# Kernel tuning notes

Measured on AMD Instinct MI355X. Metric: run time of the kernel, lower is better.

The kernel has to match this reference:

```python
import jax, jax.numpy as jnp
import numpy as np

N = 50000      # nodes
E = 800000     # directed edges (before self-loops)
IN = 128       # input feature dim
HID = 64       # per-head hidden channels (concat=False -> head mean)
H = 4          # attention heads
OUT = 1
NEG_SLOPE = 0.2


def setup_inputs() -> dict:
    key = jax.random.key(0)
    ks = jax.random.split(key, 20)
    def glorot(k, shape, fan):
        return jax.random.normal(k, shape, jnp.float32) * (1.0 / np.sqrt(fan))
    inp = {
        "x": jax.random.normal(ks[0], (N, IN), jnp.float32),
        "edge_index": jax.random.randint(ks[1], (2, E), 0, N, jnp.int32),
        # layer 1
        "W1": glorot(ks[2], (IN, H * HID), IN),
        "a_s1": glorot(ks[3], (H, HID), HID),
        "a_d1": glorot(ks[4], (H, HID), HID),
        "b1": jnp.zeros((HID,), jnp.float32),
        # layer 2
        "W2": glorot(ks[5], (HID, H * HID), HID),
        "a_s2": glorot(ks[6], (H, HID), HID),
        "a_d2": glorot(ks[7], (H, HID), HID),
        "b2": jnp.zeros((HID,), jnp.float32),
        # layer 3
        "W3": glorot(ks[8], (HID, H * HID), HID),
        "a_s3": glorot(ks[9], (H, HID), HID),
        "a_d3": glorot(ks[10], (H, HID), HID),
        "b3": jnp.zeros((HID,), jnp.float32),
        # final linear
        "fc_W": glorot(ks[11], (HID, OUT), HID),
        "fc_b": jnp.zeros((OUT,), jnp.float32),
    }
    return inp


def _gat_layer(x, src, dst, W, a_s, a_d, b):
    """PyG GATConv with concat=False (mean over heads), self-loops already in src/dst."""
    n = x.shape[0]
    h = (x @ W).reshape(n, H, -1)                      # [N,H,C]
    es = jnp.einsum('nhc,hc->nh', h, a_s)              # [N,H] alpha_src per node
    ed = jnp.einsum('nhc,hc->nh', h, a_d)              # [N,H] alpha_dst per node
    e = jax.nn.leaky_relu(es[src] + ed[dst], NEG_SLOPE)  # [E,H] per-edge logits
    # segment softmax over edges sharing the same dst (every node has a self-loop)
    m = jax.ops.segment_max(e, dst, num_segments=n)
    w = jnp.exp(e - m[dst])
    z = jax.ops.segment_sum(w, dst, num_segments=n)
    alpha = w / z[dst]                                  # [E,H]
    out = jax.ops.segment_sum(alpha[:, :, None] * h[src], dst, num_segments=n)  # [N,H,C]
    return out.mean(axis=1) + b                         # concat=False -> head mean + bias


def reference(x, edge_index, W1, a_s1, a_d1, b1, W2, a_s2, a_d2, b2,
              W3, a_s3, a_d3, b3, fc_W, fc_b):
    n = x.shape[0]
    loops = jnp.arange(n, dtype=edge_index.dtype)
    src = jnp.concatenate([edge_index[0], loops])
    dst = jnp.concatenate([edge_index[1], loops])
    gelu = lambda t: jax.nn.gelu(t, approximate=False)  # torch F.gelu default = exact erf
    x = gelu(_gat_layer(x, src, dst, W1, a_s1, a_d1, b1))
    x = gelu(_gat_layer(x, src, dst, W2, a_s2, a_d2, b2))
    x = gelu(_gat_layer(x, src, dst, W3, a_s3, a_d3, b3))
    # dropout is identity in eval mode (deterministic reference)
    return jax.nn.sigmoid(x @ fc_W + fc_b)              # [N,1]
```

## Files before the change

### kernel.cpp

```cpp
#include <hip/hip_runtime.h>
#include <math.h>

#define N_NODES 50000
#define N_EDGES 800000
#define ETOT    (N_EDGES + N_NODES)
#define DIM_IN  128
#define HID     64
#define NHEAD   4
#define HDIM    256
#define NEG_SLOPE 0.2f

typedef __attribute__((ext_vector_type(8))) short bf16x8;
typedef __attribute__((ext_vector_type(4))) float f32x4;

static __device__ __forceinline__ float gelu_exact(float x) {
    return 0.5f * x * (1.0f + erff(x * 0.70710678118654752f));
}
static __device__ __forceinline__ unsigned short f2bf(float f) {
    unsigned u = __float_as_uint(f);
    u = (u + 0x7FFFu + ((u >> 16) & 1u)) >> 16;
    return (unsigned short)u;
}
static __device__ __forceinline__ float b2f(unsigned short us) {
    return __uint_as_float(((unsigned)us) << 16);
}

__global__ void count_kernel(const int* __restrict__ ei, int* __restrict__ counts) {
    int i = blockIdx.x * 256 + threadIdx.x;
    if (i >= ETOT) return;
    int d = (i < N_EDGES) ? ei[N_EDGES + i] : (i - N_EDGES);
    atomicAdd(&counts[d], 1);
}

__global__ void scan1_kernel(const int* __restrict__ counts, int* __restrict__ offs,
                             int* __restrict__ blockSums) {
    __shared__ int s[256];
    int t = threadIdx.x, idx = blockIdx.x * 256 + t;
    int v = (idx < N_NODES) ? counts[idx] : 0;
    s[t] = v; __syncthreads();
    #pragma unroll
    for (int o = 1; o < 256; o <<= 1) {
        int add = (t >= o) ? s[t - o] : 0;
        __syncthreads();
        s[t] += add;
        __syncthreads();
    }
    if (idx < N_NODES) offs[idx] = s[t] - v;
    if (t == 255) blockSums[blockIdx.x] = s[t];
}

__global__ void scan2_kernel(const int* __restrict__ blockSums, int* __restrict__ blockScan, int nb) {
    __shared__ int s[256];
    int t = threadIdx.x;
    int v = (t < nb) ? blockSums[t] : 0;
    s[t] = v; __syncthreads();
    #pragma unroll
    for (int o = 1; o < 256; o <<= 1) {
        int add = (t >= o) ? s[t - o] : 0;
        __syncthreads();
        s[t] += add;
        __syncthreads();
    }
    blockScan[t] = s[t] - v;
}

__global__ void scan3_kernel(int* __restrict__ offs, const int* __restrict__ blockScan) {
    int idx = blockIdx.x * 256 + threadIdx.x;
    if (idx < N_NODES) offs[idx] += blockScan[blockIdx.x];
    if (idx == 0) offs[N_NODES] = ETOT;
}

__global__ void fill_kernel(const int* __restrict__ ei, const int* __restrict__ offs,
                            int* __restrict__ cursor, int* __restrict__ csrc) {
    int i = blockIdx.x * 256 + threadIdx.x;
    if (i >= ETOT) return;
    int s, d;
    if (i < N_EDGES) { s = ei[i]; d = ei[N_EDGES + i]; } else { s = d = i - N_EDGES; }
    int pos = offs[d] + atomicAdd(&cursor[d], 1);
    csrc[pos] = s;
}

__global__ void convx_kernel(const float4* __restrict__ in, ushort4* __restrict__ outp, int n4) {
    int i = blockIdx.x * 256 + threadIdx.x;
    if (i >= n4) return;
    float4 v = in[i];
    ushort4 o;
    o.x = f2bf(v.x); o.y = f2bf(v.y); o.z = f2bf(v.z); o.w = f2bf(v.w);
    outp[i] = o;
}

__global__ void convw_kernel(const float* __restrict__ W1, const float* __restrict__ W2,
                             const float* __restrict__ W3,
                             unsigned short* __restrict__ Wt1, unsigned short* __restrict__ Wt2,
                             unsigned short* __restrict__ Wt3) {
    int t = blockIdx.x * 256 + threadIdx.x;
    if (t < 32768) {
        int k = t >> 8, n = t & 255;
        Wt1[n * DIM_IN + k] = f2bf(W1[t]);
    } else if (t < 49152) {
        int l = t - 32768; int k = l >> 8, n = l & 255;
        Wt2[n * HID + k] = f2bf(W2[l]);
    } else if (t < 65536) {
        int l = t - 49152; int k = l >> 8, n = l & 255;
        Wt3[n * HID + k] = f2bf(W3[l]);
    }
}

template<int K>
__global__ __launch_bounds__(256) void gemm_mfma_kernel(
    const unsigned short* __restrict__ A, const unsigned short* __restrict__ Wt,
    const float* __restrict__ a_s, const float* __restrict__ a_d,
    unsigned short* __restrict__ h_bf, float* __restrict__ es, float* __restrict__ ed,
    int M)
{
    constexpr int KS = K / 32;
    __shared__ unsigned short hstage[64][HDIM + 8];
    const int lane = threadIdx.x & 63;
    const int head = threadIdx.x >> 6;
    const int l15 = lane & 15;
    const int lg  = lane >> 4;
    const int row0 = blockIdx.x * 64;

    bf16x8 bfrag[4][KS];
    #pragma unroll
    for (int n = 0; n < 4; ++n)
        #pragma unroll
        for (int ks = 0; ks < KS; ++ks)
            bfrag[n][ks] = *(const bf16x8*)(Wt + (size_t)(head * 64 + n * 16 + l15) * K + ks * 32 + lg * 8);

    f32x4 acc[4][4];
    #pragma unroll
    for (int m = 0; m < 4; ++m)
        #pragma unroll
        for (int n = 0; n < 4; ++n)
            acc[m][n] = (f32x4){0.f, 0.f, 0.f, 0.f};

    #pragma unroll
    for (int m = 0; m < 4; ++m) {
        int row = row0 + m * 16 + l15;
        if (row >= M) row = M - 1;
        const unsigned short* ap = A + (size_t)row * K + lg * 8;
        #pragma unroll
        for (int ks = 0; ks < KS; ++ks) {
            bf16x8 af = *(const bf16x8*)(ap + ks * 32);
            #pragma unroll
            for (int n = 0; n < 4; ++n)
                acc[m][n] = __builtin_amdgcn_mfma_f32_16x16x32_bf16(af, bfrag[n][ks], acc[m][n], 0, 0, 0);
        }
    }

    float asv[4], adv[4];
    #pragma unroll
    for (int n = 0; n < 4; ++n) {
        asv[n] = a_s[head * 64 + n * 16 + l15];
        adv[n] = a_d[head * 64 + n * 16 + l15];
    }
    #pragma unroll
    for (int m = 0; m < 4; ++m) {
        #pragma unroll
        for (int r = 0; r < 4; ++r) {
            int rloc = m * 16 + lg * 4 + r;
            float ps = 0.f, pd = 0.f;
            #pragma unroll
            for (int n = 0; n < 4; ++n) {
                float v = acc[m][n][r];
                ps += v * asv[n];
                pd += v * adv[n];
                hstage[rloc][head * 64 + n * 16 + l15] = f2bf(v);
            }
            #pragma unroll
            for (int o = 8; o; o >>= 1) { ps += __shfl_xor(ps, o, 64); pd += __shfl_xor(pd, o, 64); }
            int rg = row0 + rloc;
            if (l15 == 0 && rg < M) { es[rg * 4 + head] = ps; ed[rg * 4 + head] = pd; }
        }
    }
    __syncthreads();
    #pragma unroll
    for (int it = 0; it < 8; ++it) {
        int id = threadIdx.x + it * 256;
        int row = id >> 5, c8 = (id & 31) * 8;
        int rg = row0 + row;
        if (rg < M) {
            int4 v = *(const int4*)(&hstage[row][c8]);
            *(int4*)(h_bf + (size_t)rg * HDIM + c8) = v;
        }
    }
}

template<bool LAST>
__global__ __launch_bounds__(256) void gather_kernel(
    const unsigned short* __restrict__ h_bf,
    const float4* __restrict__ es4, const float4* __restrict__ ed4,
    const int* __restrict__ offs, const int* __restrict__ csrc,
    const float* __restrict__ bias,
    const float* __restrict__ fcW, const float* __restrict__ fcb,
    unsigned short* __restrict__ xout_bf, float* __restrict__ out)
{
    __shared__ float wls[4][64][4];
    __shared__ int   sls[4][64];
    const int wv = threadIdx.x >> 6;
    const int lane = threadIdx.x & 63;
    const int w = blockIdx.x * 4 + wv;
    const int hd = lane >> 4;
    const int ch = lane << 2;
    const int beg = offs[w], end = offs[w + 1];
    const float4 edv = ed4[w];

    float4 mx = {-INFINITY, -INFINITY, -INFINITY, -INFINITY};
    for (int i = beg + lane; i < end; i += 64) {
        float4 e = es4[csrc[i]];
        e.x += edv.x; e.y += edv.y; e.z += edv.z; e.w += edv.w;
        e.x = (e.x > 0.f) ? e.x : NEG_SLOPE * e.x;
        e.y = (e.y > 0.f) ? e.y : NEG_SLOPE * e.y;
        e.z = (e.z > 0.f) ? e.z : NEG_SLOPE * e.z;
        e.w = (e.w > 0.f) ? e.w : NEG_SLOPE * e.w;
        mx.x = fmaxf(mx.x, e.x); mx.y = fmaxf(mx.y, e.y);
        mx.z = fmaxf(mx.z, e.z); mx.w = fmaxf(mx.w, e.w);
    }
    #pragma unroll
    for (int o = 32; o; o >>= 1) {
        mx.x = fmaxf(mx.x, __shfl_xor(mx.x, o, 64));
        mx.y = fmaxf(mx.y, __shfl_xor(mx.y, o, 64));
        mx.z = fmaxf(mx.z, __shfl_xor(mx.z, o, 64));
        mx.w = fmaxf(mx.w, __shfl_xor(mx.w, o, 64));
    }

    float4 zac = {0.f, 0.f, 0.f, 0.f};
    float4 acc = {0.f, 0.f, 0.f, 0.f};
    for (int c0 = beg; c0 < end; c0 += 64) {
        int i = c0 + lane;
        float4 wt = {0.f, 0.f, 0.f, 0.f};
        int sidx = 0;
        if (i < end) {
            sidx = csrc[i];
            float4 e = es4[sidx];
            e.x += edv.x; e.y += edv.y; e.z += edv.z; e.w += edv.w;
            e.x = (e.x > 0.f) ? e.x : NEG_SLOPE * e.x;
            e.y = (e.y > 0.f) ? e.y : NEG_SLOPE * e.y;
            e.z = (e.z > 0.f) ? e.z : NEG_SLOPE * e.z;
            e.w = (e.w > 0.f) ? e.w : NEG_SLOPE * e.w;
            wt.x = __expf(e.x - mx.x); wt.y = __expf(e.y - mx.y);
            wt.z = __expf(e.z - mx.z); wt.w = __expf(e.w - mx.w);
        }
        sls[wv][lane] = sidx;
        *(float4*)(&wls[wv][lane][0]) = wt;
        zac.x += wt.x; zac.y += wt.y; zac.z += wt.z; zac.w += wt.w;
        int nb = end - c0; if (nb > 64) nb = 64;
        int j = 0;
        for (; j + 3 < nb; j += 4) {
            int s0 = sls[wv][j], s1 = sls[wv][j + 1], s2 = sls[wv][j + 2], s3 = sls[wv][j + 3];
            float a0 = wls[wv][j][hd],     a1 = wls[wv][j + 1][hd];
            float a2 = wls[wv][j + 2][hd], a3 = wls[wv][j + 3][hd];
            ushort4 u0 = *(const ushort4*)(h_bf + (size_t)s0 * HDIM + ch);
            ushort4 u1 = *(const ushort4*)(h_bf + (size_t)s1 * HDIM + ch);
            ushort4 u2 = *(const ushort4*)(h_bf + (size_t)s2 * HDIM + ch);
            ushort4 u3 = *(const ushort4*)(h_bf + (size_t)s3 * HDIM + ch);
            acc.x += a0 * b2f(u0.x) + a1 * b2f(u1.x) + a2 * b2f(u2.x) + a3 * b2f(u3.x);
            acc.y += a0 * b2f(u0.y) + a1 * b2f(u1.y) + a2 * b2f(u2.y) + a3 * b2f(u3.y);
            acc.z += a0 * b2f(u0.z) + a1 * b2f(u1.z) + a2 * b2f(u2.z) + a3 * b2f(u3.z);
            acc.w += a0 * b2f(u0.w) + a1 * b2f(u1.w) + a2 * b2f(u2.w) + a3 * b2f(u3.w);
        }
        for (; j < nb; ++j) {
            int s = sls[wv][j];
            float a = wls[wv][j][hd];
            ushort4 u = *(const ushort4*)(h_bf + (size_t)s * HDIM + ch);
            acc.x += a * b2f(u.x); acc.y += a * b2f(u.y);
            acc.z += a * b2f(u.z); acc.w += a * b2f(u.w);
        }
    }
    #pragma unroll
    for (int o = 32; o; o >>= 1) {
        zac.x += __shfl_xor(zac.x, o, 64);
        zac.y += __shfl_xor(zac.y, o, 64);
        zac.z += __shfl_xor(zac.z, o, 64);
        zac.w += __shfl_xor(zac.w, o, 64);
    }
    float zz = (hd == 0) ? zac.x : (hd == 1) ? zac.y : (hd == 2) ? zac.z : zac.w;
    float inv = 1.f / zz;
    acc.x *= inv; acc.y *= inv; acc.z *= inv; acc.w *= inv;
    acc.x += __shfl_xor(acc.x, 16, 64); acc.x += __shfl_xor(acc.x, 32, 64);
    acc.y += __shfl_xor(acc.y, 16, 64); acc.y += __shfl_xor(acc.y, 32, 64);
    acc.z += __shfl_xor(acc.z, 16, 64); acc.z += __shfl_xor(acc.z, 32, 64);
    acc.w += __shfl_xor(acc.w, 16, 64); acc.w += __shfl_xor(acc.w, 32, 64);
    if (lane < 16) {
        float4 bv = *(const float4*)(bias + ch);
        float4 r;
        r.x = gelu_exact(0.25f * acc.x + bv.x);
        r.y = gelu_exact(0.25f * acc.y + bv.y);
        r.z = gelu_exact(0.25f * acc.z + bv.z);
        r.w = gelu_exact(0.25f * acc.w + bv.w);
        if (!LAST) {
            ushort4 o4;
            o4.x = f2bf(r.x); o4.y = f2bf(r.y); o4.z = f2bf(r.z); o4.w = f2bf(r.w);
            *(ushort4*)(xout_bf + (size_t)w * HID + ch) = o4;
        } else {
            float p = r.x * fcW[ch] + r.y * fcW[ch + 1] + r.z * fcW[ch + 2] + r.w * fcW[ch + 3];
            #pragma unroll
            for (int o = 8; o; o >>= 1) p += __shfl_xor(p, o, 64);
            if (lane == 0) out[w] = 1.f / (1.f + __expf(-(p + fcb[0])));
        }
    }
}

extern "C" void kernel_launch(void* const* d_in, const int* in_sizes, int n_in,
                              void* d_out, int out_size, void* d_ws, size_t ws_size,
                              hipStream_t stream) {
    const float* x    = (const float*)d_in[0];
    const int*   ei   = (const int*)d_in[1];
    const float* W1   = (const float*)d_in[2];
    const float* as1  = (const float*)d_in[3];
    const float* ad1  = (const float*)d_in[4];
    const float* b1   = (const float*)d_in[5];
    const float* W2   = (const float*)d_in[6];
    const float* as2  = (const float*)d_in[7];
    const float* ad2  = (const float*)d_in[8];
    const float* b2   = (const float*)d_in[9];
    const float* W3   = (const float*)d_in[10];
    const float* as3  = (const float*)d_in[11];
    const float* ad3  = (const float*)d_in[12];
    const float* b3   = (const float*)d_in[13];
    const float* fcW  = (const float*)d_in[14];
    const float* fcb  = (const float*)d_in[15];
    float* out = (float*)d_out;

    char* ws = (char*)d_ws;
    size_t off = 0;
    auto alloc = [&](size_t bytes) -> void* {
        void* p = ws + off;
        off += (bytes + 255) & ~(size_t)255;
        return p;
    };
    unsigned short* h_bf  = (unsigned short*)alloc((size_t)N_NODES * HDIM * 2);
    unsigned short* x_bf  = (unsigned short*)alloc((size_t)N_NODES * DIM_IN * 2);
    unsigned short* xA_bf = (unsigned short*)alloc((size_t)N_NODES * HID * 2);
    unsigned short* xB_bf = (unsigned short*)alloc((size_t)N_NODES * HID * 2);
    unsigned short* Wt1   = (unsigned short*)alloc((size_t)HDIM * DIM_IN * 2);
    unsigned short* Wt2   = (unsigned short*)alloc((size_t)HDIM * HID * 2);
    unsigned short* Wt3   = (unsigned short*)alloc((size_t)HDIM * HID * 2);
    float* esb   = (float*)alloc((size_t)N_NODES * 4 * 4);
    float* edb   = (float*)alloc((size_t)N_NODES * 4 * 4);
    int* offs    = (int*)alloc((size_t)(N_NODES + 1) * 4);
    int* counts  = (int*)alloc((size_t)2 * N_NODES * 4);
    int* cursor  = counts + N_NODES;
    int* bsums   = (int*)alloc(256 * 4);
    int* bscan   = (int*)alloc(256 * 4);
    int* csrc    = (int*)alloc((size_t)ETOT * 4);

    const int NB    = (N_NODES + 255) / 256;
    const int EB    = (ETOT + 255) / 256;
    const int GB    = (N_NODES + 63) / 64;
    const int AGB   = N_NODES / 4;
    const int CXB   = (N_NODES * DIM_IN / 4 + 255) / 256;

    hipMemsetAsync(counts, 0, (size_t)2 * N_NODES * 4, stream);
    count_kernel<<<EB, 256, 0, stream>>>(ei, counts);
    scan1_kernel<<<NB, 256, 0, stream>>>(counts, offs, bsums);
    scan2_kernel<<<1, 256, 0, stream>>>(bsums, bscan, NB);
    scan3_kernel<<<NB, 256, 0, stream>>>(offs, bscan);
    fill_kernel<<<EB, 256, 0, stream>>>(ei, offs, cursor, csrc);

    convx_kernel<<<CXB, 256, 0, stream>>>((const float4*)x, (ushort4*)x_bf, N_NODES * DIM_IN / 4);
    convw_kernel<<<256, 256, 0, stream>>>(W1, W2, W3, Wt1, Wt2, Wt3);

    gemm_mfma_kernel<DIM_IN><<<GB, 256, 0, stream>>>(x_bf, Wt1, as1, ad1, h_bf, esb, edb, N_NODES);
    gather_kernel<false><<<AGB, 256, 0, stream>>>(h_bf, (const float4*)esb, (const float4*)edb,
                                                  offs, csrc, b1, fcW, fcb, xA_bf, out);
    gemm_mfma_kernel<HID><<<GB, 256, 0, stream>>>(xA_bf, Wt2, as2, ad2, h_bf, esb, edb, N_NODES);
    gather_kernel<false><<<AGB, 256, 0, stream>>>(h_bf, (const float4*)esb, (const float4*)edb,
                                                  offs, csrc, b2, fcW, fcb, xB_bf, out);
    gemm_mfma_kernel<HID><<<GB, 256, 0, stream>>>(xB_bf, Wt3, as3, ad3, h_bf, esb, edb, N_NODES);
    gather_kernel<true><<<AGB, 256, 0, stream>>>(h_bf, (const float4*)esb, (const float4*)edb,
                                                 offs, csrc, b3, fcW, fcb, xA_bf, out);
}
```

Before: 461.4 us.

## Fuse CSR build into cooperative prep kernel and restructure gather aggregation

The memset, count, three scan, fill and two bf16-conversion launches are merged into one cooperative kernel that uses grid-wide syncs between phases. This cuts launch overhead and inter-kernel gaps. The CSR now stores pre-scaled byte offsets (src<<9), so row addresses come straight from the stored value. The gather kernel gains a single-pass path for nodes with degree up to 64, which skips the separate max pass. It also has each half-wave load 16-byte chunks for two edges at a time, which means fewer, wider h loads and less redundant score gathering. The cost is cooperative-launch constraints and more register use for the 8-wide accumulators.

```diff
diff --git a/kernel.cpp b/kernel.cpp
--- a/kernel.cpp
+++ b/kernel.cpp
@@ -1,4 +1,5 @@
 #include <hip/hip_runtime.h>
+#include <hip/hip_cooperative_groups.h>
 #include <math.h>
 
 #define N_NODES 50000
@@ -21,88 +22,89 @@
     u = (u + 0x7FFFu + ((u >> 16) & 1u)) >> 16;
     return (unsigned short)u;
 }
-static __device__ __forceinline__ float b2f(unsigned short us) {
-    return __uint_as_float(((unsigned)us) << 16);
-}
-
-__global__ void count_kernel(const int* __restrict__ ei, int* __restrict__ counts) {
-    int i = blockIdx.x * 256 + threadIdx.x;
-    if (i >= ETOT) return;
-    int d = (i < N_EDGES) ? ei[N_EDGES + i] : (i - N_EDGES);
-    atomicAdd(&counts[d], 1);
-}
-
-__global__ void scan1_kernel(const int* __restrict__ counts, int* __restrict__ offs,
-                             int* __restrict__ blockSums) {
-    __shared__ int s[256];
-    int t = threadIdx.x, idx = blockIdx.x * 256 + t;
-    int v = (idx < N_NODES) ? counts[idx] : 0;
-    s[t] = v; __syncthreads();
-    #pragma unroll
-    for (int o = 1; o < 256; o <<= 1) {
-        int add = (t >= o) ? s[t - o] : 0;
-        __syncthreads();
-        s[t] += add;
-        __syncthreads();
-    }
-    if (idx < N_NODES) offs[idx] = s[t] - v;
-    if (t == 255) blockSums[blockIdx.x] = s[t];
-}
-
-__global__ void scan2_kernel(const int* __restrict__ blockSums, int* __restrict__ blockScan, int nb) {
-    __shared__ int s[256];
-    int t = threadIdx.x;
-    int v = (t < nb) ? blockSums[t] : 0;
-    s[t] = v; __syncthreads();
-    #pragma unroll
-    for (int o = 1; o < 256; o <<= 1) {
-        int add = (t >= o) ? s[t - o] : 0;
-        __syncthreads();
-        s[t] += add;
-        __syncthreads();
-    }
-    blockScan[t] = s[t] - v;
-}
-
-__global__ void scan3_kernel(int* __restrict__ offs, const int* __restrict__ blockScan) {
-    int idx = blockIdx.x * 256 + threadIdx.x;
-    if (idx < N_NODES) offs[idx] += blockScan[blockIdx.x];
-    if (idx == 0) offs[N_NODES] = ETOT;
-}
-
-__global__ void fill_kernel(const int* __restrict__ ei, const int* __restrict__ offs,
-                            int* __restrict__ cursor, int* __restrict__ csrc) {
-    int i = blockIdx.x * 256 + threadIdx.x;
-    if (i >= ETOT) return;
-    int s, d;
-    if (i < N_EDGES) { s = ei[i]; d = ei[N_EDGES + i]; } else { s = d = i - N_EDGES; }
-    int pos = offs[d] + atomicAdd(&cursor[d], 1);
-    csrc[pos] = s;
-}
-
-__global__ void convx_kernel(const float4* __restrict__ in, ushort4* __restrict__ outp, int n4) {
-    int i = blockIdx.x * 256 + threadIdx.x;
-    if (i >= n4) return;
-    float4 v = in[i];
-    ushort4 o;
-    o.x = f2bf(v.x); o.y = f2bf(v.y); o.z = f2bf(v.z); o.w = f2bf(v.w);
-    outp[i] = o;
-}
-
-__global__ void convw_kernel(const float* __restrict__ W1, const float* __restrict__ W2,
-                             const float* __restrict__ W3,
-                             unsigned short* __restrict__ Wt1, unsigned short* __restrict__ Wt2,
-                             unsigned short* __restrict__ Wt3) {
-    int t = blockIdx.x * 256 + threadIdx.x;
-    if (t < 32768) {
-        int k = t >> 8, n = t & 255;
-        Wt1[n * DIM_IN + k] = f2bf(W1[t]);
-    } else if (t < 49152) {
-        int l = t - 32768; int k = l >> 8, n = l & 255;
-        Wt2[n * HID + k] = f2bf(W2[l]);
-    } else if (t < 65536) {
-        int l = t - 49152; int k = l >> 8, n = l & 255;
-        Wt3[n * HID + k] = f2bf(W3[l]);
+
+__global__ void prep_kernel(
+    const float* __restrict__ x, const int* __restrict__ ei,
+    const float* __restrict__ W1, const float* __restrict__ W2, const float* __restrict__ W3,
+    unsigned short* __restrict__ x_bf,
+    unsigned short* __restrict__ Wt1, unsigned short* __restrict__ Wt2, unsigned short* __restrict__ Wt3,
+    int* __restrict__ counts,
+    int* __restrict__ offs, int* __restrict__ bsums, int* __restrict__ bscan,
+    int* __restrict__ coff)
+{
+    cooperative_groups::grid_group grid = cooperative_groups::this_grid();
+    __shared__ int sblk[256];
+    const int tid  = blockIdx.x * 256 + threadIdx.x;
+    const int nthr = 256 * 256;
+
+    for (int t = tid; t < 65536; t += nthr) {
+        if (t < 32768) {
+            int k = t >> 8, n = t & 255;
+            Wt1[n * DIM_IN + k] = f2bf(W1[t]);
+        } else if (t < 49152) {
+            int l = t - 32768; int k = l >> 8, n = l & 255;
+            Wt2[n * HID + k] = f2bf(W2[l]);
+        } else {
+            int l = t - 49152; int k = l >> 8, n = l & 255;
+            Wt3[n * HID + k] = f2bf(W3[l]);
+        }
+    }
+    for (int i = tid; i < N_NODES * DIM_IN / 4; i += nthr) {
+        float4 v = ((const float4*)x)[i];
+        ushort4 o;
+        o.x = f2bf(v.x); o.y = f2bf(v.y); o.z = f2bf(v.z); o.w = f2bf(v.w);
+        ((ushort4*)x_bf)[i] = o;
+    }
+    for (int i = tid; i < 2 * N_NODES; i += nthr) counts[i] = 0;
+    grid.sync();
+
+    for (int i = tid; i < ETOT; i += nthr) {
+        int d = (i < N_EDGES) ? ei[N_EDGES + i] : (i - N_EDGES);
+        atomicAdd(&counts[d], 1);
+    }
+    grid.sync();
+
+    if (blockIdx.x < 196) {
+        int t = threadIdx.x, idx = blockIdx.x * 256 + t;
+        int v = (idx < N_NODES) ? counts[idx] : 0;
+        sblk[t] = v; __syncthreads();
+        #pragma unroll
+        for (int o = 1; o < 256; o <<= 1) {
+            int add = (t >= o) ? sblk[t - o] : 0;
+            __syncthreads();
+            sblk[t] += add;
+            __syncthreads();
+        }
+        if (idx < N_NODES) offs[idx] = sblk[t] - v;
+        if (t == 255) bsums[blockIdx.x] = sblk[t];
+    }
+    grid.sync();
+
+    if (blockIdx.x == 0) {
+        int t = threadIdx.x;
+        int v = (t < 196) ? bsums[t] : 0;
+        sblk[t] = v; __syncthreads();
+        #pragma unroll
+        for (int o = 1; o < 256; o <<= 1) {
+            int add = (t >= o) ? sblk[t - o] : 0;
+            __syncthreads();
+            sblk[t] += add;
+            __syncthreads();
+        }
+        bscan[t] = sblk[t] - v;
+    }
+    grid.sync();
+
+    for (int i = tid; i < N_NODES; i += nthr) offs[i] += bscan[i >> 8];
+    if (tid == 0) offs[N_NODES] = ETOT;
+    grid.sync();
+
+    int* cursor = counts + N_NODES;
+    for (int i = tid; i < ETOT; i += nthr) {
+        int s, d;
+        if (i < N_EDGES) { s = ei[i]; d = ei[N_EDGES + i]; } else { s = d = i - N_EDGES; }
+        int pos = offs[d] + atomicAdd(&cursor[d], 1);
+        coff[pos] = s << 9;
     }
 }
 
@@ -187,87 +189,152 @@
     }
 }
 
+static __device__ __forceinline__ float4 lrelu4(float4 e) {
+    e.x = (e.x > 0.f) ? e.x : NEG_SLOPE * e.x;
+    e.y = (e.y > 0.f) ? e.y : NEG_SLOPE * e.y;
+    e.z = (e.z > 0.f) ? e.z : NEG_SLOPE * e.z;
+    e.w = (e.w > 0.f) ? e.w : NEG_SLOPE * e.w;
+    return e;
+}
+
 template<bool LAST>
 __global__ __launch_bounds__(256) void gather_kernel(
     const unsigned short* __restrict__ h_bf,
     const float4* __restrict__ es4, const float4* __restrict__ ed4,
-    const int* __restrict__ offs, const int* __restrict__ csrc,
+    const int* __restrict__ offs, const int* __restrict__ coff,
     const float* __restrict__ bias,
     const float* __restrict__ fcW, const float* __restrict__ fcb,
     unsigned short* __restrict__ xout_bf, float* __restrict__ out)
 {
-    __shared__ float wls[4][64][4];
+    __shared__ float wls[4][4][72];
     __shared__ int   sls[4][64];
-    const int wv = threadIdx.x >> 6;
+    const int wv   = threadIdx.x >> 6;
     const int lane = threadIdx.x & 63;
-    const int w = blockIdx.x * 4 + wv;
-    const int hd = lane >> 4;
-    const int ch = lane << 2;
+    const int w    = blockIdx.x * 4 + wv;
+    const int l32  = lane & 31;
+    const int half = lane >> 5;
+    const int hd8  = l32 >> 3;
     const int beg = offs[w], end = offs[w + 1];
+    const int deg = end - beg;
     const float4 edv = ed4[w];
-
-    float4 mx = {-INFINITY, -INFINITY, -INFINITY, -INFINITY};
-    for (int i = beg + lane; i < end; i += 64) {
-        float4 e = es4[csrc[i]];
-        e.x += edv.x; e.y += edv.y; e.z += edv.z; e.w += edv.w;
-        e.x = (e.x > 0.f) ? e.x : NEG_SLOPE * e.x;
-        e.y = (e.y > 0.f) ? e.y : NEG_SLOPE * e.y;
-        e.z = (e.z > 0.f) ? e.z : NEG_SLOPE * e.z;
-        e.w = (e.w > 0.f) ? e.w : NEG_SLOPE * e.w;
-        mx.x = fmaxf(mx.x, e.x); mx.y = fmaxf(mx.y, e.y);
-        mx.z = fmaxf(mx.z, e.z); mx.w = fmaxf(mx.w, e.w);
-    }
-    #pragma unroll
-    for (int o = 32; o; o >>= 1) {
-        mx.x = fmaxf(mx.x, __shfl_xor(mx.x, o, 64));
-        mx.y = fmaxf(mx.y, __shfl_xor(mx.y, o, 64));
-        mx.z = fmaxf(mx.z, __shfl_xor(mx.z, o, 64));
-        mx.w = fmaxf(mx.w, __shfl_xor(mx.w, o, 64));
-    }
-
+    const char* hch = (const char*)h_bf + l32 * 16;
+
+    float acc[8];
+    #pragma unroll
+    for (int c = 0; c < 8; ++c) acc[c] = 0.f;
     float4 zac = {0.f, 0.f, 0.f, 0.f};
-    float4 acc = {0.f, 0.f, 0.f, 0.f};
-    for (int c0 = beg; c0 < end; c0 += 64) {
-        int i = c0 + lane;
+
+    if (deg <= 64) {
+        float4 e = {-INFINITY, -INFINITY, -INFINITY, -INFINITY};
+        int sb = 0;
+        if (lane < deg) {
+            sb = coff[beg + lane];
+            float4 ev = *(const float4*)((const char*)es4 + (((unsigned)sb) >> 5));
+            ev.x += edv.x; ev.y += edv.y; ev.z += edv.z; ev.w += edv.w;
+            e = lrelu4(ev);
+        }
+        float4 mx = e;
+        #pragma unroll
+        for (int o = 32; o; o >>= 1) {
+            mx.x = fmaxf(mx.x, __shfl_xor(mx.x, o, 64));
+            mx.y = fmaxf(mx.y, __shfl_xor(mx.y, o, 64));
+            mx.z = fmaxf(mx.z, __shfl_xor(mx.z, o, 64));
+            mx.w = fmaxf(mx.w, __shfl_xor(mx.w, o, 64));
+        }
         float4 wt = {0.f, 0.f, 0.f, 0.f};
-        int sidx = 0;
-        if (i < end) {
-            sidx = csrc[i];
-            float4 e = es4[sidx];
-            e.x += edv.x; e.y += edv.y; e.z += edv.z; e.w += edv.w;
-            e.x = (e.x > 0.f) ? e.x : NEG_SLOPE * e.x;
-            e.y = (e.y > 0.f) ? e.y : NEG_SLOPE * e.y;
-            e.z = (e.z > 0.f) ? e.z : NEG_SLOPE * e.z;
-            e.w = (e.w > 0.f) ? e.w : NEG_SLOPE * e.w;
+        if (lane < deg) {
             wt.x = __expf(e.x - mx.x); wt.y = __expf(e.y - mx.y);
             wt.z = __expf(e.z - mx.z); wt.w = __expf(e.w - mx.w);
         }
-        sls[wv][lane] = sidx;
-        *(float4*)(&wls[wv][lane][0]) = wt;
-        zac.x += wt.x; zac.y += wt.y; zac.z += wt.z; zac.w += wt.w;
-        int nb = end - c0; if (nb > 64) nb = 64;
-        int j = 0;
-        for (; j + 3 < nb; j += 4) {
-            int s0 = sls[wv][j], s1 = sls[wv][j + 1], s2 = sls[wv][j + 2], s3 = sls[wv][j + 3];
-            float a0 = wls[wv][j][hd],     a1 = wls[wv][j + 1][hd];
-            float a2 = wls[wv][j + 2][hd], a3 = wls[wv][j + 3][hd];
-            ushort4 u0 = *(const ushort4*)(h_bf + (size_t)s0 * HDIM + ch);
-            ushort4 u1 = *(const ushort4*)(h_bf + (size_t)s1 * HDIM + ch);
-            ushort4 u2 = *(const ushort4*)(h_bf + (size_t)s2 * HDIM + ch);
-            ushort4 u3 = *(const ushort4*)(h_bf + (size_t)s3 * HDIM + ch);
-            acc.x += a0 * b2f(u0.x) + a1 * b2f(u1.x) + a2 * b2f(u2.x) + a3 * b2f(u3.x);
-            acc.y += a0 * b2f(u0.y) + a1 * b2f(u1.y) + a2 * b2f(u2.y) + a3 * b2f(u3.y);
-            acc.z += a0 * b2f(u0.z) + a1 * b2f(u1.z) + a2 * b2f(u2.z) + a3 * b2f(u3.z);
-            acc.w += a0 * b2f(u0.w) + a1 * b2f(u1.w) + a2 * b2f(u2.w) + a3 * b2f(u3.w);
-        }
-        for (; j < nb; ++j) {
-            int s = sls[wv][j];
-            float a = wls[wv][j][hd];
-            ushort4 u = *(const ushort4*)(h_bf + (size_t)s * HDIM + ch);
-            acc.x += a * b2f(u.x); acc.y += a * b2f(u.y);
-            acc.z += a * b2f(u.z); acc.w += a * b2f(u.w);
-        }
-    }
+        sls[wv][lane] = sb;
+        wls[wv][0][lane] = wt.x; wls[wv][1][lane] = wt.y;
+        wls[wv][2][lane] = wt.z; wls[wv][3][lane] = wt.w;
+        zac = wt;
+        for (int j = 0; j < deg; j += 4) {
+            int j0 = j + half, j1 = j + 2 + half;
+            int o0 = sls[wv][j0], o1 = sls[wv][j1];
+            float a0 = wls[wv][hd8][j0], a1 = wls[wv][hd8][j1];
+            int4 u0 = *(const int4*)(hch + o0);
+            int4 u1 = *(const int4*)(hch + o1);
+            acc[0] += a0 * __uint_as_float(((unsigned)u0.x) << 16);
+            acc[1] += a0 * __uint_as_float(u0.x & 0xffff0000u);
+            acc[2] += a0 * __uint_as_float(((unsigned)u0.y) << 16);
+            acc[3] += a0 * __uint_as_float(u0.y & 0xffff0000u);
+            acc[4] += a0 * __uint_as_float(((unsigned)u0.z) << 16);
+            acc[5] += a0 * __uint_as_float(u0.z & 0xffff0000u);
+            acc[6] += a0 * __uint_as_float(((unsigned)u0.w) << 16);
+            acc[7] += a0 * __uint_as_float(u0.w & 0xffff0000u);
+            acc[0] += a1 * __uint_as_float(((unsigned)u1.x) << 16);
+            acc[1] += a1 * __uint_as_float(u1.x & 0xffff0000u);
+            acc[2] += a1 * __uint_as_float(((unsigned)u1.y) << 16);
+            acc[3] += a1 * __uint_as_float(u1.y & 0xffff0000u);
+            acc[4] += a1 * __uint_as_float(((unsigned)u1.z) << 16);
+            acc[5] += a1 * __uint_as_float(u1.z & 0xffff0000u);
+            acc[6] += a1 * __uint_as_float(((unsigned)u1.w) << 16);
+            acc[7] += a1 * __uint_as_float(u1.w & 0xffff0000u);
+        }
+    } else {
+        float4 mx = {-INFINITY, -INFINITY, -INFINITY, -INFINITY};
+        for (int i = beg + lane; i < end; i += 64) {
+            int sb = coff[i];
+            float4 ev = *(const float4*)((const char*)es4 + (((unsigned)sb) >> 5));
+            ev.x += edv.x; ev.y += edv.y; ev.z += edv.z; ev.w += edv.w;
+            ev = lrelu4(ev);
+            mx.x = fmaxf(mx.x, ev.x); mx.y = fmaxf(mx.y, ev.y);
+            mx.z = fmaxf(mx.z, ev.z); mx.w = fmaxf(mx.w, ev.w);
+        }
+        #pragma unroll
+        for (int o = 32; o; o >>= 1) {
+            mx.x = fmaxf(mx.x, __shfl_xor(mx.x, o, 64));
+            mx.y = fmaxf(mx.y, __shfl_xor(mx.y, o, 64));
+            mx.z = fmaxf(mx.z, __shfl_xor(mx.z, o, 64));
+            mx.w = fmaxf(mx.w, __shfl_xor(mx.w, o, 64));
+        }
+        for (int c0 = beg; c0 < end; c0 += 64) {
+            int i = c0 + lane;
+            float4 wt = {0.f, 0.f, 0.f, 0.f};
+            int sb = 0;
+            if (i < end) {
+                sb = coff[i];
+                float4 ev = *(const float4*)((const char*)es4 + (((unsigned)sb) >> 5));
+                ev.x += edv.x; ev.y += edv.y; ev.z += edv.z; ev.w += edv.w;
+                ev = lrelu4(ev);
+                wt.x = __expf(ev.x - mx.x); wt.y = __expf(ev.y - mx.y);
+                wt.z = __expf(ev.z - mx.z); wt.w = __expf(ev.w - mx.w);
+            }
+            sls[wv][lane] = sb;
+            wls[wv][0][lane] = wt.x; wls[wv][1][lane] = wt.y;
+            wls[wv][2][lane] = wt.z; wls[wv][3][lane] = wt.w;
+            zac.x += wt.x; zac.y += wt.y; zac.z += wt.z; zac.w += wt.w;
+            int nb = end - c0; if (nb > 64) nb = 64;
+            for (int j = 0; j < nb; j += 4) {
+                int j0 = j + half, j1 = j + 2 + half;
+                int o0 = sls[wv][j0], o1 = sls[wv][j1];
+                float a0 = wls[wv][hd8][j0], a1 = wls[wv][hd8][j1];
+                int4 u0 = *(const int4*)(hch + o0);
+                int4 u1 = *(const int4*)(hch + o1);
+                acc[0] += a0 * __uint_as_float(((unsigned)u0.x) << 16);
+                acc[1] += a0 * __uint_as_float(u0.x & 0xffff0000u);
+                acc[2] += a0 * __uint_as_float(((unsigned)u0.y) << 16);
+                acc[3] += a0 * __uint_as_float(u0.y & 0xffff0000u);
+                acc[4] += a0 * __uint_as_float(((unsigned)u0.z) << 16);
+                acc[5] += a0 * __uint_as_float(u0.z & 0xffff0000u);
+                acc[6] += a0 * __uint_as_float(((unsigned)u0.w) << 16);
+                acc[7] += a0 * __uint_as_float(u0.w & 0xffff0000u);
+                acc[0] += a1 * __uint_as_float(((unsigned)u1.x) << 16);
+                acc[1] += a1 * __uint_as_float(u1.x & 0xffff0000u);
+                acc[2] += a1 * __uint_as_float(((unsigned)u1.y) << 16);
+                acc[3] += a1 * __uint_as_float(u1.y & 0xffff0000u);
+                acc[4] += a1 * __uint_as_float(((unsigned)u1.z) << 16);
+                acc[5] += a1 * __uint_as_float(u1.z & 0xffff0000u);
+                acc[6] += a1 * __uint_as_float(((unsigned)u1.w) << 16);
+                acc[7] += a1 * __uint_as_float(u1.w & 0xffff0000u);
+            }
+        }
+    }
+
+    #pragma unroll
+    for (int c = 0; c < 8; ++c) acc[c] += __shfl_xor(acc[c], 32, 64);
     #pragma unroll
     for (int o = 32; o; o >>= 1) {
         zac.x += __shfl_xor(zac.x, o, 64);
@@ -275,30 +342,45 @@
         zac.z += __shfl_xor(zac.z, o, 64);
         zac.w += __shfl_xor(zac.w, o, 64);
     }
-    float zz = (hd == 0) ? zac.x : (hd == 1) ? zac.y : (hd == 2) ? zac.z : zac.w;
+    float zz = (hd8 == 0) ? zac.x : (hd8 == 1) ? zac.y : (hd8 == 2) ? zac.z : zac.w;
     float inv = 1.f / zz;
-    acc.x *= inv; acc.y *= inv; acc.z *= inv; acc.w *= inv;
-    acc.x += __shfl_xor(acc.x, 16, 64); acc.x += __shfl_xor(acc.x, 32, 64);
-    acc.y += __shfl_xor(acc.y, 16, 64); acc.y += __shfl_xor(acc.y, 32, 64);
-    acc.z += __shfl_xor(acc.z, 16, 64); acc.z += __shfl_xor(acc.z, 32, 64);
-    acc.w += __shfl_xor(acc.w, 16, 64); acc.w += __shfl_xor(acc.w, 32, 64);
-    if (lane < 16) {
-        float4 bv = *(const float4*)(bias + ch);
-        float4 r;
-        r.x = gelu_exact(0.25f * acc.x + bv.x);
-        r.y = gelu_exact(0.25f * acc.y + bv.y);
-        r.z = gelu_exact(0.25f * acc.z + bv.z);
-        r.w = gelu_exact(0.25f * acc.w + bv.w);
-        if (!LAST) {
-            ushort4 o4;
-            o4.x = f2bf(r.x); o4.y = f2bf(r.y); o4.z = f2bf(r.z); o4.w = f2bf(r.w);
-            *(ushort4*)(xout_bf + (size_t)w * HID + ch) = o4;
-        } else {
-            float p = r.x * fcW[ch] + r.y * fcW[ch + 1] + r.z * fcW[ch + 2] + r.w * fcW[ch + 3];
-            #pragma unroll
-            for (int o = 8; o; o >>= 1) p += __shfl_xor(p, o, 64);
-            if (lane == 0) out[w] = 1.f / (1.f + __expf(-(p + fcb[0])));
-        }
+    #pragma unroll
+    for (int c = 0; c < 8; ++c) acc[c] *= inv;
+    #pragma unroll
+    for (int c = 0; c < 8; ++c) {
+        acc[c] += __shfl_xor(acc[c], 8, 64);
+        acc[c] += __shfl_xor(acc[c], 16, 64);
+    }
+    const int d0 = (l32 & 7) * 8;
+    float4 b0 = *(const float4*)(bias + d0);
+    float4 b1 = *(const float4*)(bias + d0 + 4);
+    float r[8];
+    r[0] = gelu_exact(0.25f * acc[0] + b0.x);
+    r[1] = gelu_exact(0.25f * acc[1] + b0.y);
+    r[2] = gelu_exact(0.25f * acc[2] + b0.z);
+    r[3] = gelu_exact(0.25f * acc[3] + b0.w);
+    r[4] = gelu_exact(0.25f * acc[4] + b1.x);
+    r[5] = gelu_exact(0.25f * acc[5] + b1.y);
+    r[6] = gelu_exact(0.25f * acc[6] + b1.z);
+    r[7] = gelu_exact(0.25f * acc[7] + b1.w);
+    if (!LAST) {
+        if (lane < 8) {
+            int4 o4;
+            o4.x = (int)((((unsigned)f2bf(r[1])) << 16) | f2bf(r[0]));
+            o4.y = (int)((((unsigned)f2bf(r[3])) << 16) | f2bf(r[2]));
+            o4.z = (int)((((unsigned)f2bf(r[5])) << 16) | f2bf(r[4]));
+            o4.w = (int)((((unsigned)f2bf(r[7])) << 16) | f2bf(r[6]));
+            *(int4*)(xout_bf + w * HID + d0) = o4;
+        }
+    } else {
+        float4 f0 = *(const float4*)(fcW + d0);
+        float4 f1 = *(const float4*)(fcW + d0 + 4);
+        float p = r[0]*f0.x + r[1]*f0.y + r[2]*f0.z + r[3]*f0.w
+                + r[4]*f1.x + r[5]*f1.y + r[6]*f1.z + r[7]*f1.w;
+        p += __shfl_xor(p, 1, 64);
+        p += __shfl_xor(p, 2, 64);
+        p += __shfl_xor(p, 4, 64);
+        if (lane == 0) out[w] = 1.f / (1.f + __expf(-(p + fcb[0])));
     }
 }
 
@@ -341,34 +423,27 @@
     float* edb   = (float*)alloc((size_t)N_NODES * 4 * 4);
     int* offs    = (int*)alloc((size_t)(N_NODES + 1) * 4);
     int* counts  = (int*)alloc((size_t)2 * N_NODES * 4);
-    int* cursor  = counts + N_NODES;
     int* bsums   = (int*)alloc(256 * 4);
     int* bscan   = (int*)alloc(256 * 4);
-    int* csrc    = (int*)alloc((size_t)ETOT * 4);
-
-    const int NB    = (N_NODES + 255) / 256;
-    const int EB    = (ETOT + 255) / 256;
-    const int GB    = (N_NODES + 63) / 64;
-    const int AGB   = N_NODES / 4;
-    const int CXB   = (N_NODES * DIM_IN / 4 + 255) / 256;
-
-    hipMemsetAsync(counts, 0, (size_t)2 * N_NODES * 4, stream);
-    count_kernel<<<EB, 256, 0, stream>>>(ei, counts);
-    scan1_kernel<<<NB, 256, 0, stream>>>(counts, offs, bsums);
-    scan2_kernel<<<1, 256, 0, stream>>>(bsums, bscan, NB);
-    scan3_kernel<<<NB, 256, 0, stream>>>(offs, bscan);
-    fill_kernel<<<EB, 256, 0, stream>>>(ei, offs, cursor, csrc);
-
-    convx_kernel<<<CXB, 256, 0, stream>>>((const float4*)x, (ushort4*)x_bf, N_NODES * DIM_IN / 4);
-    convw_kernel<<<256, 256, 0, stream>>>(W1, W2, W3, Wt1, Wt2, Wt3);
+    int* coff    = (int*)alloc((size_t)ETOT * 4);
+
+    const int GB  = (N_NODES + 63) / 64;
+    const int AGB = N_NODES / 4;
+
+    void* args[] = {
+        (void*)&x, (void*)&ei, (void*)&W1, (void*)&W2, (void*)&W3,
+        (void*)&x_bf, (void*)&Wt1, (void*)&Wt2, (void*)&Wt3,
+        (void*)&counts, (void*)&offs, (void*)&bsums, (void*)&bscan, (void*)&coff
+    };
+    hipLaunchCooperativeKernel((void*)prep_kernel, dim3(256), dim3(256), args, 0, stream);
 
     gemm_mfma_kernel<DIM_IN><<<GB, 256, 0, stream>>>(x_bf, Wt1, as1, ad1, h_bf, esb, edb, N_NODES);
     gather_kernel<false><<<AGB, 256, 0, stream>>>(h_bf, (const float4*)esb, (const float4*)edb,
-                                                  offs, csrc, b1, fcW, fcb, xA_bf, out);
+                                                  offs, coff, b1, fcW, fcb, xA_bf, out);
     gemm_mfma_kernel<HID><<<GB, 256, 0, stream>>>(xA_bf, Wt2, as2, ad2, h_bf, esb, edb, N_NODES);
     gather_kernel<false><<<AGB, 256, 0, stream>>>(h_bf, (const float4*)esb, (const float4*)edb,
-                                                  offs, csrc, b2, fcW, fcb, xB_bf, out);
+                                                  offs, coff, b2, fcW, fcb, xB_bf, out);
     gemm_mfma_kernel<HID><<<GB, 256, 0, stream>>>(xB_bf, Wt3, as3, ad3, h_bf, esb, edb, N_NODES);
     gather_kernel<true><<<AGB, 256, 0, stream>>>(h_bf, (const float4*)esb, (const float4*)edb,
-                                                 offs, csrc, b3, fcW, fcb, xA_bf, out);
-}
+                                                 offs, coff, b3, fcW, fcb, xA_bf, out);
+}
```

Measured after the change: 612.7 us. +32.8%, slower.
